# Kernel tuning notes

Measured on AMD Instinct MI355X. Metric: run time of the kernel, lower is better.

Reference implementation:

```python
import jax, jax.numpy as jnp
import numpy as np

N_GRAPHS = 1250
NEG_SLOPE = 0.2

def gat_layer(x, src, dst, W, a_src, a_dst, b, concat):
    # x: [N, Fin]; W: [Fin, H*C]; a_src/a_dst: [H, C]; b: [H*C] or [C]
    N = x.shape[0]
    H, C = a_src.shape
    h = (x @ W).reshape(N, H, C)                      # [N,H,C]
    alpha_s = jnp.sum(h * a_src[None], axis=-1)       # [N,H]
    alpha_d = jnp.sum(h * a_dst[None], axis=-1)       # [N,H]
    e = jax.nn.leaky_relu(alpha_s[src] + alpha_d[dst], NEG_SLOPE)  # [E,H]
    # segment softmax over incoming edges of each target node
    m = jax.ops.segment_max(e, dst, num_segments=N)   # [N,H]
    m = jnp.where(jnp.isfinite(m), m, 0.0)
    ex = jnp.exp(e - m[dst])
    s = jax.ops.segment_sum(ex, dst, num_segments=N)  # [N,H]
    alpha = ex / (s[dst] + 1e-16)                     # [E,H]
    msg = h[src] * alpha[..., None]                   # [E,H,C]
    out = jax.ops.segment_sum(msg, dst, num_segments=N)  # [N,H,C]
    out = out.reshape(N, H * C) if concat else out.mean(axis=1)
    return out + b

def setup_inputs() -> dict:
    key = jax.random.key(0)
    ks = jax.random.split(key, 13)
    N, E = 50000, 100000
    x = jax.random.normal(ks[0], (N, 78), dtype=jnp.float32)
    edge_index = jax.random.randint(ks[1], (2, E), 0, N, dtype=jnp.int64)
    # sorted segment ids -> every graph non-empty (~40 nodes each)
    batch = jnp.sort(jax.random.randint(ks[2], (N,), 0, N_GRAPHS, dtype=jnp.int64))
    g = lambda k, shape, fan: jax.random.normal(k, shape, dtype=jnp.float32) / np.float32(np.sqrt(fan))
    return {
        'x': x, 'edge_index': edge_index, 'batch': batch,
        'W1': g(ks[3], (78, 780), 78), 'a_src1': g(ks[4], (10, 78), 78), 'a_dst1': g(ks[5], (10, 78), 78),
        'b1': jnp.zeros((780,), jnp.float32),
        'W2': g(ks[6], (780, 128), 780), 'a_src2': g(ks[7], (1, 128), 128), 'a_dst2': g(ks[8], (1, 128), 128),
        'b2': jnp.zeros((128,), jnp.float32),
        'fc_w': g(ks[9], (128, 128), 128), 'fc_b': jnp.zeros((128,), jnp.float32),
    }

def reference(x, edge_index, batch, W1, a_src1, a_dst1, b1, W2, a_src2, a_dst2, b2, fc_w, fc_b):
    N = x.shape[0]
    loop = jnp.arange(N, dtype=edge_index.dtype)
    src = jnp.concatenate([edge_index[0], loop])  # add self loops (PyG default)
    dst = jnp.concatenate([edge_index[1], loop])
    # dropout layers are identity in eval mode
    h = jax.nn.elu(gat_layer(x, src, dst, W1, a_src1, a_dst1, b1, concat=True))   # [N,780]
    h = jax.nn.relu(gat_layer(h, src, dst, W2, a_src2, a_dst2, b2, concat=True))  # [N,128]
    g = jax.ops.segment_max(h, batch, num_segments=N_GRAPHS)                      # [G,128]
    g = jnp.where(jnp.isfinite(g), g, 0.0)
    return jax.nn.relu(g @ fc_w + fc_b)
```

## Files before the change

### kernel.cpp

```cpp
#include <hip/hip_runtime.h>
#include <hip/hip_bf16.h>
#include <cstdint>

#define CAP 32
typedef __hip_bfloat16 bf16;
typedef __attribute__((ext_vector_type(8))) short short8;
typedef __attribute__((ext_vector_type(4))) float f32x4;

__device__ __forceinline__ float sb2f(short s) {
  unsigned int u = ((unsigned int)(unsigned short)s) << 16;
  return __uint_as_float(u);
}
__device__ __forceinline__ short f2sb(float f) {
  bf16 h = __float2bfloat16(f);
  return *reinterpret_cast<short*>(&h);
}

__global__ void k_detect(const int* __restrict__ ei, int* __restrict__ flag) {
  __shared__ int any;
  if (threadIdx.x == 0) any = 0;
  __syncthreads();
  int v = 0;
  for (int i = 1 + 2 * threadIdx.x; i < 2000; i += 512) v |= ei[i];
  if (v) atomicOr(&any, 1);
  __syncthreads();
  if (threadIdx.x == 0) flag[0] = (any == 0) ? 1 : 0;
}

__device__ __forceinline__ void edge_sd(const int* __restrict__ ei, int e, int f,
                                        int& src, int& dst) {
  if (e < 100000) {
    if (f) { src = ei[2 * e]; dst = ei[200000 + 2 * e]; }
    else   { src = ei[e];     dst = ei[100000 + e]; }
  } else { src = dst = e - 100000; }
  src = min(max(src, 0), 49999);
  dst = min(max(dst, 0), 49999);
}

__global__ void k_prep(const float* __restrict__ x, const float* __restrict__ W1,
                       const float* __restrict__ W2, const float* __restrict__ aw1,
                       const float* __restrict__ dw1, bf16* __restrict__ xb,
                       bf16* __restrict__ W1t, bf16* __restrict__ W2t,
                       bf16* __restrict__ Wat, float* __restrict__ zp, int zeroWords) {
  int i = blockIdx.x * 256 + threadIdx.x;
  if (i < zeroWords) zp[i] = 0.f;
  const int n_xb = 50000 * 96;
  const int n_w1 = 832 * 96;
  const int n_w2 = 128 * 832;
  const int n_wa = 32 * 96;
  if (i < n_xb) {
    int r = i / 96, k = i - r * 96;
    xb[i] = __float2bfloat16(k < 78 ? x[r * 78 + k] : 0.f);
  } else if (i < n_xb + n_w1) {
    int j = i - n_xb;
    int n = j / 96, k = j - n * 96;
    W1t[j] = __float2bfloat16((k < 78 && n < 780) ? W1[k * 780 + n] : 0.f);
  } else if (i < n_xb + n_w1 + n_w2) {
    int j = i - n_xb - n_w1;
    int c = j / 832, k = j - c * 832;
    W2t[j] = __float2bfloat16(k < 780 ? W2[k * 128 + c] : 0.f);
  } else if (i < n_xb + n_w1 + n_w2 + n_wa) {
    int j = i - n_xb - n_w1 - n_w2;
    int c = j / 96, k = j - c * 96;
    float s = 0.f;
    if (k < 78 && c < 20) {
      const float* w = (c < 10) ? aw1 : dw1;
      int h = (c < 10) ? c : c - 10;
      const float* wrow = W1 + k * 780 + h * 78;
      const float* arow = w + h * 78;
      for (int q = 0; q < 78; q++) s += wrow[q] * arow[q];
    }
    Wat[c * 96 + k] = __float2bfloat16(s);
  }
}

__global__ __launch_bounds__(256) void k_gemm1(const bf16* __restrict__ xb,
                                               const bf16* __restrict__ W1t,
                                               const bf16* __restrict__ Wat,
                                               const float* __restrict__ b1,
                                               bf16* __restrict__ H1,
                                               float* __restrict__ as1,
                                               float* __restrict__ ad1) {
  __shared__ __align__(16) short Als[64 * 104];
  __shared__ __align__(16) short Bls[64 * 104];
  __shared__ __align__(16) short Wls[32 * 104];
  __shared__ __align__(16) float Cls[64 * 68];
  __shared__ float b1s[832];
  const int t = threadIdx.x;
  const int w = t >> 6, l = t & 63, l15 = l & 15, q = l >> 4;
  const int rowBase = blockIdx.x * 64;
  for (int s = t; s < 768; s += 256) {
    int row = s / 12, kg = s - row * 12;
    short8 v = {};
    int gr = rowBase + row;
    if (gr < 50000) v = *(const short8*)((const short*)xb + (size_t)gr * 96 + kg * 8);
    *(short8*)&Als[row * 104 + kg * 8] = v;
  }
  for (int s = t; s < 384; s += 256) {
    int row = s / 12, kg = s - row * 12;
    *(short8*)&Wls[row * 104 + kg * 8] =
        *(const short8*)((const short*)Wat + (size_t)row * 96 + kg * 8);
  }
  for (int s = t; s < 832; s += 256) b1s[s] = (s < 780) ? b1[s] : 0.f;
  short8 breg[3];
  int bn[3], bk[3];
#pragma unroll
  for (int i = 0; i < 3; i++) {
    int s = t + i * 256;
    bn[i] = s / 12; bk[i] = s - bn[i] * 12;
    breg[i] = *(const short8*)((const short*)W1t + (size_t)bn[i] * 96 + bk[i] * 8);
  }
  for (int cc = 0; cc < 13; cc++) {
    __syncthreads();
#pragma unroll
    for (int i = 0; i < 3; i++) *(short8*)&Bls[bn[i] * 104 + bk[i] * 8] = breg[i];
    if (cc < 12) {
#pragma unroll
      for (int i = 0; i < 3; i++)
        breg[i] = *(const short8*)((const short*)W1t +
                                   (size_t)((cc + 1) * 64 + bn[i]) * 96 + bk[i] * 8);
    }
    __syncthreads();
    f32x4 acc[4] = {};
#pragma unroll
    for (int ks = 0; ks < 3; ks++) {
      short8 a = *(const short8*)&Als[(w * 16 + l15) * 104 + ks * 32 + q * 8];
#pragma unroll
      for (int nt = 0; nt < 4; nt++) {
        short8 b = *(const short8*)&Bls[(nt * 16 + l15) * 104 + ks * 32 + q * 8];
        acc[nt] = __builtin_amdgcn_mfma_f32_16x16x32_bf16(a, b, acc[nt], 0, 0, 0);
      }
    }
    __syncthreads();
#pragma unroll
    for (int nt = 0; nt < 4; nt++)
#pragma unroll
      for (int r = 0; r < 4; r++)
        Cls[(w * 16 + q * 4 + r) * 68 + nt * 16 + l15] = acc[nt][r];
    __syncthreads();
    {
      int r = t >> 2, c0 = (t & 3) * 16;
      int gr = rowBase + r;
      if (gr < 50000) {
        short8 o0, o1;
#pragma unroll
        for (int c = 0; c < 8; c++) o0[c] = f2sb(Cls[r * 68 + c0 + c] + b1s[cc * 64 + c0 + c]);
#pragma unroll
        for (int c = 0; c < 8; c++) o1[c] = f2sb(Cls[r * 68 + c0 + 8 + c] + b1s[cc * 64 + c0 + 8 + c]);
        short* dst = (short*)H1 + (size_t)gr * 832 + cc * 64 + c0;
        *(short8*)dst = o0;
        *(short8*)(dst + 8) = o1;
      }
    }
  }
  f32x4 acc2[2] = {};
#pragma unroll
  for (int ks = 0; ks < 3; ks++) {
    short8 a = *(const short8*)&Als[(w * 16 + l15) * 104 + ks * 32 + q * 8];
#pragma unroll
    for (int nt = 0; nt < 2; nt++) {
      short8 b = *(const short8*)&Wls[(nt * 16 + l15) * 104 + ks * 32 + q * 8];
      acc2[nt] = __builtin_amdgcn_mfma_f32_16x16x32_bf16(a, b, acc2[nt], 0, 0, 0);
    }
  }
  const int gr0 = rowBase + w * 16 + q * 4;
#pragma unroll
  for (int nt = 0; nt < 2; nt++) {
    int c = nt * 16 + l15;
#pragma unroll
    for (int r = 0; r < 4; r++) {
      int gr = gr0 + r;
      if (gr < 50000) {
        if (c < 10)       as1[gr * 10 + c] = acc2[nt][r];
        else if (c < 20)  ad1[gr * 10 + (c - 10)] = acc2[nt][r];
      }
    }
  }
}

__global__ void k_scatter(const int* __restrict__ ei, const int* __restrict__ flag,
                          int* __restrict__ cnt, int* __restrict__ csr) {
  int e = blockIdx.x * 256 + threadIdx.x;
  if (e >= 150000) return;
  int f = flag[0], src, dst;
  edge_sd(ei, e, f, src, dst);
  int pos = atomicAdd(&cnt[dst], 1);
  if (pos < CAP) csr[dst * CAP + pos] = src;
}

__global__ __launch_bounds__(256) void k_agg1(const bf16* __restrict__ H1,
                                              const float* __restrict__ as1,
                                              const float* __restrict__ ad1,
                                              const int* __restrict__ csr,
                                              const int* __restrict__ cnt,
                                              bf16* __restrict__ HL2) {
  __shared__ float sexw[2][CAP * 10];
  __shared__ float sden[2][16];
  __shared__ int ssrc[2][CAP];
  __shared__ int scnt[2];
  const int t = threadIdx.x;
  const int sub = t >> 7, tt = t & 127;
  const int n = blockIdx.x * 2 + sub;
  if (t < 2) scnt[t] = min(cnt[blockIdx.x * 2 + t], CAP);
  if (t >= 32 && t < 64) { int z = t - 32; sden[z >> 4][z & 15] = 0.f; }
  __syncthreads();
  const int cn = scnt[sub];
  if (tt < cn) ssrc[sub][tt] = csr[n * CAP + tt];
  __syncthreads();
  for (int wv = tt; wv < cn * 10; wv += 128) {
    int k = wv / 10, h = wv - k * 10;
    int src = ssrc[sub][k];
    float e = as1[src * 10 + h] + ad1[n * 10 + h];
    e = e >= 0.f ? e : 0.2f * e;
    float ex = __expf(e);
    sexw[sub][wv] = ex;
    atomicAdd(&sden[sub][h], ex);
  }
  __syncthreads();
  if (tt < 104) {
    const int j0 = tt * 8;
    int hj[8];
#pragma unroll
    for (int c = 0; c < 8; c++) {
      int h = (j0 + c) / 78;
      hj[c] = h > 9 ? 9 : h;
    }
    float acc[8] = {};
    const float* sw = sexw[sub];
    const short* H1s = (const short*)H1;
    for (int k = 0; k < cn; k++) {
      int src = ssrc[sub][k];
      short8 hv = *(const short8*)(H1s + (size_t)src * 832 + j0);
      const float* swk = sw + k * 10;
#pragma unroll
      for (int c = 0; c < 8; c++) acc[c] += swk[hj[c]] * sb2f(hv[c]);
    }
    const int hsplit = (j0 / 78 + 1) * 78 - j0;
    const float r0 = 1.f / (sden[sub][hj[0]] + 1e-16f);
    const float r1 = 1.f / (sden[sub][hj[7]] + 1e-16f);
    short8 ov;
#pragma unroll
    for (int c = 0; c < 8; c++) {
      float v = acc[c] * (c < hsplit ? r0 : r1);
      v = v > 0.f ? v : __expf(v) - 1.f;
      ov[c] = f2sb(v);
    }
    *(short8*)((short*)HL2 + (size_t)n * 832 + j0) = ov;
  }
}

__global__ __launch_bounds__(256) void k_gemm2(const bf16* __restrict__ A,
                                               const bf16* __restrict__ W2t,
                                               const float* __restrict__ AW2,
                                               const float* __restrict__ DW2,
                                               bf16* __restrict__ H2,
                                               float* __restrict__ as2,
                                               float* __restrict__ ad2) {
  __shared__ __align__(16) short Als[64 * 72];
  __shared__ __align__(16) short Bls[128 * 72];
  __shared__ float sAW[128], sDW[128];
  __shared__ float sS[4][64], sD[4][64];
  const int t = threadIdx.x;
  const int w = t >> 6, l = t & 63, l15 = l & 15, q = l >> 4;
  const int rowBase = blockIdx.x * 64;
  if (t < 128) sAW[t] = AW2[t];
  else         sDW[t - 128] = DW2[t - 128];
  const int ar = t >> 2, ak = t & 3;
  short8 areg[2], breg[4];
  {
    int gr0 = rowBase + ar;
#pragma unroll
    for (int i = 0; i < 2; i++) {
      short8 v = {};
      int gr = gr0;
      if (gr < 50000)
        v = *(const short8*)((const short*)A + (size_t)gr * 832 + 0 + (ak * 2 + i) * 8);
      areg[i] = v;
    }
#pragma unroll
    for (int i = 0; i < 4; i++) {
      int s = t + i * 256;
      int col = s >> 3, kg = s & 7;
      breg[i] = *(const short8*)((const short*)W2t + (size_t)col * 832 + 0 + kg * 8);
    }
  }
  f32x4 acc[4][2] = {};
  for (int kb = 0; kb < 832; kb += 64) {
    __syncthreads();
#pragma unroll
    for (int i = 0; i < 2; i++)
      *(short8*)&Als[ar * 72 + (ak * 2 + i) * 8] = areg[i];
#pragma unroll
    for (int i = 0; i < 4; i++) {
      int s = t + i * 256;
      int col = s >> 3, kg = s & 7;
      *(short8*)&Bls[col * 72 + kg * 8] = breg[i];
    }
    if (kb < 768) {
      int kn = kb + 64;
      int gr = rowBase + ar;
#pragma unroll
      for (int i = 0; i < 2; i++) {
        short8 v = {};
        if (gr < 50000)
          v = *(const short8*)((const short*)A + (size_t)gr * 832 + kn + (ak * 2 + i) * 8);
        areg[i] = v;
      }
#pragma unroll
      for (int i = 0; i < 4; i++) {
        int s = t + i * 256;
        int col = s >> 3, kg = s & 7;
        breg[i] = *(const short8*)((const short*)W2t + (size_t)col * 832 + kn + kg * 8);
      }
    }
    __syncthreads();
#pragma unroll
    for (int ks = 0; ks < 2; ks++) {
      short8 a[4];
#pragma unroll
      for (int mt = 0; mt < 4; mt++)
        a[mt] = *(const short8*)&Als[(mt * 16 + l15) * 72 + ks * 32 + q * 8];
#pragma unroll
      for (int ntl = 0; ntl < 2; ntl++) {
        short8 b = *(const short8*)&Bls[((w * 2 + ntl) * 16 + l15) * 72 + ks * 32 + q * 8];
#pragma unroll
        for (int mt = 0; mt < 4; mt++)
          acc[mt][ntl] = __builtin_amdgcn_mfma_f32_16x16x32_bf16(a[mt], b, acc[mt][ntl], 0, 0, 0);
      }
    }
  }
  const int col0 = w * 32 + l15, col1 = col0 + 16;
  const float aw0 = sAW[col0], aw1 = sAW[col1];
  const float dw0 = sDW[col0], dw1 = sDW[col1];
  f32x4 sp[4], dp[4];
#pragma unroll
  for (int mt = 0; mt < 4; mt++) {
    sp[mt] = acc[mt][0] * aw0 + acc[mt][1] * aw1;
    dp[mt] = acc[mt][0] * dw0 + acc[mt][1] * dw1;
  }
#pragma unroll
  for (int m = 1; m < 16; m <<= 1) {
#pragma unroll
    for (int mt = 0; mt < 4; mt++)
#pragma unroll
      for (int r = 0; r < 4; r++) {
        sp[mt][r] += __shfl_xor(sp[mt][r], m, 64);
        dp[mt][r] += __shfl_xor(dp[mt][r], m, 64);
      }
  }
  if (l15 == 0) {
#pragma unroll
    for (int mt = 0; mt < 4; mt++)
#pragma unroll
      for (int r = 0; r < 4; r++) {
        sS[w][mt * 16 + q * 4 + r] = sp[mt][r];
        sD[w][mt * 16 + q * 4 + r] = dp[mt][r];
      }
  }
#pragma unroll
  for (int mt = 0; mt < 4; mt++) {
    int gr0 = rowBase + mt * 16 + q * 4;
#pragma unroll
    for (int ntl = 0; ntl < 2; ntl++) {
      int gc = w * 32 + ntl * 16 + l15;
#pragma unroll
      for (int r = 0; r < 4; r++) {
        int gr = gr0 + r;
        if (gr < 50000) H2[(size_t)gr * 128 + gc] = __float2bfloat16(acc[mt][ntl][r]);
      }
    }
  }
  __syncthreads();
  if (t < 64) {
    int gr = rowBase + t;
    if (gr < 50000) as2[gr] = sS[0][t] + sS[1][t] + sS[2][t] + sS[3][t];
  } else if (t < 128) {
    int r2 = t - 64;
    int gr = rowBase + r2;
    if (gr < 50000) ad2[gr] = sD[0][r2] + sD[1][r2] + sD[2][r2] + sD[3][r2];
  }
}

__global__ __launch_bounds__(128) void k_agg2(const bf16* __restrict__ H2,
                                              const float* __restrict__ as2,
                                              const float* __restrict__ ad2,
                                              const int* __restrict__ csr,
                                              const int* __restrict__ cnt,
                                              const float* __restrict__ b2,
                                              const int* __restrict__ batch,
                                              const int* __restrict__ flag,
                                              float* __restrict__ g) {
  __shared__ int ssrc[CAP];
  __shared__ float sexw[CAP];
  __shared__ float sden;
  __shared__ int scnt, sbv;
  const int t = threadIdx.x;
  const int n = blockIdx.x;
  if (t == 0) {
    scnt = min(cnt[n], CAP);
    sden = 0.f;
    int b = flag[0] ? batch[2 * n] : batch[n];
    sbv = min(max(b, 0), 1249);
  }
  __syncthreads();
  const int cn = scnt;
  if (t < cn) {
    int src = csr[n * CAP + t];
    ssrc[t] = src;
    float e = as2[src] + ad2[n];
    e = e >= 0.f ? e : 0.2f * e;
    float ex = __expf(e);
    sexw[t] = ex;
    atomicAdd(&sden, ex);
  }
  __syncthreads();
  const short* H2s = (const short*)H2;
  float acc = 0.f;
  if (cn > 0) {
    short hv = H2s[(size_t)ssrc[0] * 128 + t];
    for (int k = 0; k < cn; k++) {
      short hn = hv;
      if (k + 1 < cn) hn = H2s[(size_t)ssrc[k + 1] * 128 + t];
      acc += sexw[k] * sb2f(hv);
      hv = hn;
    }
  }
  float v = acc / (sden + 1e-16f) + b2[t];
  v = v > 0.f ? v : 0.f;
  atomicMax((int*)&g[sbv * 128 + t], __float_as_int(v));
}

__global__ __launch_bounds__(128) void k_fc(const float* __restrict__ g,
                                            const float* __restrict__ fw,
                                            const float* __restrict__ fb,
                                            float* __restrict__ out) {
  const int n = blockIdx.x, t = threadIdx.x;
  __shared__ float grow[128];
  grow[t] = g[n * 128 + t];
  __syncthreads();
  float acc = fb[t];
  for (int k = 0; k < 128; k++) acc += grow[k] * fw[k * 128 + t];
  out[n * 128 + t] = acc > 0.f ? acc : 0.f;
}

extern "C" void kernel_launch(void* const* d_in, const int* in_sizes, int n_in,
                              void* d_out, int out_size, void* d_ws, size_t ws_size,
                              hipStream_t stream) {
  const float* x     = (const float*)d_in[0];
  const int*   ei    = (const int*)d_in[1];
  const int*   batch = (const int*)d_in[2];
  const float* W1    = (const float*)d_in[3];
  const float* as1w  = (const float*)d_in[4];
  const float* ad1w  = (const float*)d_in[5];
  const float* b1    = (const float*)d_in[6];
  const float* W2    = (const float*)d_in[7];
  const float* as2w  = (const float*)d_in[8];
  const float* ad2w  = (const float*)d_in[9];
  const float* b2    = (const float*)d_in[10];
  const float* fcw   = (const float*)d_in[11];
  const float* fcb   = (const float*)d_in[12];
  float* out = (float*)d_out;

  char* p = (char*)d_ws;
  size_t off = 0;
  auto alloc = [&](size_t bytes) -> void* {
    void* r = p + off;
    off = (off + bytes + 15) & ~(size_t)15;
    return r;
  };
  int*   cnt = (int*)  alloc(50000 * 4);
  float* g   = (float*)alloc(160000 * 4);
  size_t zeroWords = off / 4;
  float* as1 = (float*)alloc(500000 * 4);
  float* ad1 = (float*)alloc(500000 * 4);
  float* as2 = (float*)alloc(50000 * 4);
  float* ad2 = (float*)alloc(50000 * 4);
  bf16*  W1t = (bf16*) alloc((size_t)832 * 96 * 2);
  bf16*  W2t = (bf16*) alloc((size_t)128 * 832 * 2);
  bf16*  Wat = (bf16*) alloc((size_t)32 * 96 * 2);
  bf16*  h1  = (bf16*) alloc((size_t)50000 * 832 * 2);
  bf16*  hl2 = (bf16*) alloc((size_t)50000 * 832 * 2);
  int*   csr = (int*)  alloc((size_t)50000 * CAP * 4);
  void*  uni = alloc((size_t)50000 * 128 * 2);
  bf16*  xb  = (bf16*)uni;
  bf16*  h2  = (bf16*)uni;
  int*   flag = (int*) alloc(16);
  (void)ws_size; (void)in_sizes; (void)n_in; (void)out_size;

  k_detect<<<1, 256, 0, stream>>>(ei, flag);
  int prepN = 50000 * 96 + 832 * 96 + 128 * 832 + 32 * 96;
  k_prep<<<(prepN + 255) / 256, 256, 0, stream>>>(
      x, W1, W2, as1w, ad1w, xb, W1t, W2t, Wat, (float*)d_ws, (int)zeroWords);

  k_gemm1<<<782, 256, 0, stream>>>(xb, W1t, Wat, b1, h1, as1, ad1);
  k_scatter<<<(150000 + 255) / 256, 256, 0, stream>>>(ei, flag, cnt, csr);
  k_agg1<<<25000, 256, 0, stream>>>(h1, as1, ad1, csr, cnt, hl2);
  k_gemm2<<<782, 256, 0, stream>>>(hl2, W2t, as2w, ad2w, h2, as2, ad2);
  k_agg2<<<50000, 128, 0, stream>>>(h2, as2, ad2, csr, cnt, b2, batch, flag, g);
  k_fc<<<1250, 128, 0, stream>>>(g, fcw, fcb, out);
}
```

Baseline: 282.4 us.

## Pad each attention head to 80 columns so 8-wide chunks never straddle heads

Changes the layer-1 feature layout so each of the 10 heads occupies 80 padded columns instead of 78 contiguous ones. W1t, W2t and the bias are permuted to match. In the aggregation kernel every 8-element chunk now belongs to a single head, so one attention weight and one denominator are loaded per edge instead of a per-element head lookup and split handling. The trade is slightly more zero padding in the GEMMs and an extra store that writes the padded tail columns as zeros.

```diff
diff --git a/kernel.cpp b/kernel.cpp
--- a/kernel.cpp
+++ b/kernel.cpp
@@ -15,6 +15,7 @@
   bf16 h = __float2bfloat16(f);
   return *reinterpret_cast<short*>(&h);
 }
+
 
 __global__ void k_detect(const int* __restrict__ ei, int* __restrict__ flag) {
   __shared__ int any;
@@ -52,16 +53,22 @@
     int r = i / 96, k = i - r * 96;
     xb[i] = __float2bfloat16(k < 78 ? x[r * 78 + k] : 0.f);
   } else if (i < n_xb + n_w1) {
-    int j = i - n_xb;
-    int n = j / 96, k = j - n * 96;
-    W1t[j] = __float2bfloat16((k < 78 && n < 780) ? W1[k * 780 + n] : 0.f);
+    int jdx = i - n_xb;
+    int np = jdx / 96, k = jdx - np * 96;
+    int h = np / 80, j = np - h * 80;
+    float v = 0.f;
+    if (k < 78 && np < 800 && j < 78) v = W1[k * 780 + (h * 78 + j)];
+    W1t[jdx] = __float2bfloat16(v);
   } else if (i < n_xb + n_w1 + n_w2) {
-    int j = i - n_xb - n_w1;
-    int c = j / 832, k = j - c * 832;
-    W2t[j] = __float2bfloat16(k < 780 ? W2[k * 128 + c] : 0.f);
+    int jdx = i - n_xb - n_w1;
+    int c = jdx / 832, kp = jdx - c * 832;
+    int h = kp / 80, j = kp - h * 80;
+    float v = 0.f;
+    if (kp < 800 && j < 78) v = W2[(h * 78 + j) * 128 + c];
+    W2t[jdx] = __float2bfloat16(v);
   } else if (i < n_xb + n_w1 + n_w2 + n_wa) {
-    int j = i - n_xb - n_w1 - n_w2;
-    int c = j / 96, k = j - c * 96;
+    int jdx = i - n_xb - n_w1 - n_w2;
+    int c = jdx / 96, k = jdx - c * 96;
     float s = 0.f;
     if (k < 78 && c < 20) {
       const float* w = (c < 10) ? aw1 : dw1;
@@ -101,7 +108,10 @@
     *(short8*)&Wls[row * 104 + kg * 8] =
         *(const short8*)((const short*)Wat + (size_t)row * 96 + kg * 8);
   }
-  for (int s = t; s < 832; s += 256) b1s[s] = (s < 780) ? b1[s] : 0.f;
+  for (int s = t; s < 832; s += 256) {
+    int h = s / 80, j = s - h * 80;
+    b1s[s] = (s < 800 && j < 78) ? b1[h * 78 + j] : 0.f;
+  }
   short8 breg[3];
   int bn[3], bk[3];
 #pragma unroll
@@ -217,35 +227,31 @@
     atomicAdd(&sden[sub][h], ex);
   }
   __syncthreads();
-  if (tt < 104) {
+  if (tt < 100) {
+    const int head = tt / 10;
     const int j0 = tt * 8;
-    int hj[8];
-#pragma unroll
-    for (int c = 0; c < 8; c++) {
-      int h = (j0 + c) / 78;
-      hj[c] = h > 9 ? 9 : h;
-    }
     float acc[8] = {};
-    const float* sw = sexw[sub];
+    const float* sw = sexw[sub] + head;
     const short* H1s = (const short*)H1;
     for (int k = 0; k < cn; k++) {
       int src = ssrc[sub][k];
       short8 hv = *(const short8*)(H1s + (size_t)src * 832 + j0);
-      const float* swk = sw + k * 10;
-#pragma unroll
-      for (int c = 0; c < 8; c++) acc[c] += swk[hj[c]] * sb2f(hv[c]);
-    }
-    const int hsplit = (j0 / 78 + 1) * 78 - j0;
-    const float r0 = 1.f / (sden[sub][hj[0]] + 1e-16f);
-    const float r1 = 1.f / (sden[sub][hj[7]] + 1e-16f);
+      float wk = sw[k * 10];
+#pragma unroll
+      for (int c = 0; c < 8; c++) acc[c] += wk * sb2f(hv[c]);
+    }
+    const float r0 = 1.f / (sden[sub][head] + 1e-16f);
     short8 ov;
 #pragma unroll
     for (int c = 0; c < 8; c++) {
-      float v = acc[c] * (c < hsplit ? r0 : r1);
+      float v = acc[c] * r0;
       v = v > 0.f ? v : __expf(v) - 1.f;
       ov[c] = f2sb(v);
     }
     *(short8*)((short*)HL2 + (size_t)n * 832 + j0) = ov;
+  } else if (tt < 104) {
+    short8 z = {};
+    *(short8*)((short*)HL2 + (size_t)n * 832 + tt * 8) = z;
   }
 }
 
```

After: 278.7 us. No clear change (-1.3%).
